# Kernel tuning notes

Hardware: AMD Instinct MI355X
Metric: run time of the kernel (lower is better)

Reference implementation:

```python
import jax, jax.numpy as jnp
import numpy as np

B, T, C, H = 4, 2048, 1024, 16
D = C // H  # head_dim = 64

def setup_inputs() -> dict:
    key = jax.random.key(0)
    k1, k2, k3 = jax.random.split(key, 3)
    x = jax.random.normal(k1, (B, T, C), dtype=jnp.float32)
    # Linear weights stored as (out_features, in_features) like torch; we apply x @ W.T
    w_attn = jax.random.normal(k2, (3 * C, C), dtype=jnp.float32) * (1.0 / np.sqrt(C))
    w_proj = jax.random.normal(k3, (C, C), dtype=jnp.float32) * (1.0 / np.sqrt(C))
    return {"x": x, "w_attn": w_attn, "w_proj": w_proj}

def reference(x, w_attn, w_proj):
    Bv, Tv, Cv = x.shape
    qkv = jnp.einsum('btc,fc->btf', x, w_attn)  # [B,T,3C]
    q, k, v = jnp.split(qkv, 3, axis=-1)
    # [B,H,T,D]
    q = q.reshape(Bv, Tv, H, D).transpose(0, 2, 1, 3)
    k = k.reshape(Bv, Tv, H, D).transpose(0, 2, 1, 3)
    v = v.reshape(Bv, Tv, H, D).transpose(0, 2, 1, 3)
    scale = 1.0 / np.sqrt(D).astype(np.float32)
    att = jnp.einsum('bhqd,bhkd->bhqk', q, k) * scale
    causal = jnp.tril(jnp.ones((Tv, Tv), dtype=bool))
    att = jnp.where(causal, att, -jnp.inf)
    att = jax.nn.softmax(att, axis=-1)
    y = jnp.einsum('bhqk,bhkd->bhqd', att, v)
    y = y.transpose(0, 2, 1, 3).reshape(Bv, Tv, Cv)
    return jnp.einsum('btc,oc->bto', y, w_proj)
```

## Files before the change

kernel.cpp:

```cpp
#include <hip/hip_runtime.h>
#include <cstdint>
#include <cstddef>

typedef __attribute__((ext_vector_type(8))) short short8;
typedef __attribute__((ext_vector_type(4))) float f32x4;
typedef unsigned int u32;

#define MFMA_BF16(a, b, c) __builtin_amdgcn_mfma_f32_16x16x32_bf16((a), (b), (c), 0, 0, 0)

__device__ __forceinline__ void async16(const void* g, void* l) {
  __builtin_amdgcn_global_load_lds(
      (const __attribute__((address_space(1))) u32*)g,
      (__attribute__((address_space(3))) u32*)l, 16, 0, 0);
}

__device__ __forceinline__ short f2bf(float f) {
  u32 u = __builtin_bit_cast(u32, f);
  u += 0x7fffu + ((u >> 16) & 1u);
  return (short)(u >> 16);
}

__device__ __forceinline__ u32 pack_bf16_trunc(float lo, float hi) {
  return __builtin_amdgcn_perm(__builtin_bit_cast(u32, hi),
                               __builtin_bit_cast(u32, lo), 0x07060302u);
}

__global__ void cast_bf16_kernel(const float* __restrict__ in,
                                 short* __restrict__ out, int n4) {
  int i = blockIdx.x * blockDim.x + threadIdx.x;
  if (i < n4) {
    float4 v = ((const float4*)in)[i];
    short4 r;
    r.x = f2bf(v.x); r.y = f2bf(v.y); r.z = f2bf(v.z); r.w = f2bf(v.w);
    ((short4*)out)[i] = r;
  }
}

__global__ void cast_wattn_kernel(const float* __restrict__ in,
                                  short* __restrict__ out, int n4) {
  int i = blockIdx.x * blockDim.x + threadIdx.x;
  if (i < n4) {
    const float sc = (i * 4 < 1024 * 1024) ? 0.18033688011112042f : 1.0f;
    float4 v = ((const float4*)in)[i];
    short4 r;
    r.x = f2bf(v.x * sc); r.y = f2bf(v.y * sc);
    r.z = f2bf(v.z * sc); r.w = f2bf(v.w * sc);
    ((short4*)out)[i] = r;
  }
}

template <bool OUT_BF16>
__global__ __launch_bounds__(256) void gemm_bt_kernel(
    const short* __restrict__ A, const short* __restrict__ Bt,
    void* __restrict__ Cv, int M, int N, int K) {
  __shared__ __align__(16) short As[128 * 32];
  __shared__ __align__(16) short Bs[128 * 32];

  const int tid  = threadIdx.x;
  const int lane = tid & 63;
  const int wave = tid >> 6;
  const int quad = lane >> 4;
  const int l15  = lane & 15;
  const int bm   = blockIdx.y * 128;
  const int bn   = blockIdx.x * 128;
  const int wm   = (wave >> 1) * 64;
  const int wn   = (wave & 1) * 64;

  f32x4 acc[4][4];
#pragma unroll
  for (int i = 0; i < 4; ++i)
#pragma unroll
    for (int j = 0; j < 4; ++j) acc[i][j] = (f32x4){0.f, 0.f, 0.f, 0.f};

  const int ci0 = tid, ci1 = tid + 256;
  const short* ga0 = A  + (size_t)(bm + (ci0 >> 2)) * K + (ci0 & 3) * 8;
  const short* ga1 = A  + (size_t)(bm + (ci1 >> 2)) * K + (ci1 & 3) * 8;
  const short* gb0 = Bt + (size_t)(bn + (ci0 >> 2)) * K + (ci0 & 3) * 8;
  const short* gb1 = Bt + (size_t)(bn + (ci1 >> 2)) * K + (ci1 & 3) * 8;

  for (int k0 = 0; k0 < K; k0 += 32) {
    __syncthreads();
    async16(ga0 + k0, &As[ci0 * 8]);
    async16(ga1 + k0, &As[ci1 * 8]);
    async16(gb0 + k0, &Bs[ci0 * 8]);
    async16(gb1 + k0, &Bs[ci1 * 8]);
    __syncthreads();

    short8 af[4], bf[4];
#pragma unroll
    for (int mt = 0; mt < 4; ++mt)
      af[mt] = *(const short8*)&As[(wm + mt * 16 + l15) * 32 + quad * 8];
#pragma unroll
    for (int nt = 0; nt < 4; ++nt)
      bf[nt] = *(const short8*)&Bs[(wn + nt * 16 + l15) * 32 + quad * 8];
#pragma unroll
    for (int mt = 0; mt < 4; ++mt)
#pragma unroll
      for (int nt = 0; nt < 4; ++nt)
        acc[mt][nt] = MFMA_BF16(af[mt], bf[nt], acc[mt][nt]);
  }

#pragma unroll
  for (int mt = 0; mt < 4; ++mt) {
    const int r0 = bm + wm + mt * 16 + quad * 4;
#pragma unroll
    for (int nt = 0; nt < 4; ++nt) {
      const int c = bn + wn + nt * 16 + l15;
#pragma unroll
      for (int reg = 0; reg < 4; ++reg) {
        float v = acc[mt][nt][reg];
        if (OUT_BF16)
          ((short*)Cv)[(size_t)(r0 + reg) * N + c] = f2bf(v);
        else
          ((float*)Cv)[(size_t)(r0 + reg) * N + c] = v;
      }
    }
  }
}

__global__ __launch_bounds__(256) void vtrans_kernel(
    const short* __restrict__ qkv, short* __restrict__ vt) {
  __shared__ __align__(16) short Ts[64 * 80];
  const int t0 = blockIdx.x * 64;
  const int bh = blockIdx.y;
  const int b = bh >> 4, h = bh & 15;
  const int tid = threadIdx.x;
#pragma unroll
  for (int it = 0; it < 2; ++it) {
    const int ci = tid + it * 256;
    const int t = ci >> 3, cw = ci & 7;
    short8 v = *(const short8*)(qkv + (size_t)(b * 2048 + t0 + t) * 3072 +
                                2048 + h * 64 + cw * 8);
    *(short8*)&Ts[t * 80 + cw * 8] = v;
  }
  __syncthreads();
#pragma unroll
  for (int it = 0; it < 2; ++it) {
    const int ci = tid + it * 256;
    const int d = ci >> 3, c2 = ci & 7;
    short tmp[8];
#pragma unroll
    for (int j = 0; j < 8; ++j) tmp[j] = Ts[(c2 * 8 + j) * 80 + d];
    *(short8*)(vt + (size_t)(bh * 64 + d) * 2048 + t0 + c2 * 8) =
        *(short8*)tmp;
  }
}

__global__ __launch_bounds__(256, 2) void attn_kernel(
    const short* __restrict__ qkv, const short* __restrict__ vt,
    short* __restrict__ y) {
  __shared__ __align__(16) short Ks[2][2 * 64 * 32];
  __shared__ __align__(16) short Vs[2][2 * 64 * 32];
  __shared__ __align__(16) short Ps[4][1024];

  const int bh    = blockIdx.x;
  const int pairi = blockIdx.y;
  const int b = bh >> 4, h = bh & 15;
  const int tid  = threadIdx.x;
  const int lane = tid & 63;
  const int wave = tid >> 6;
  const int quad = lane >> 4, l15 = lane & 15;
  const int base_row = b * 2048;
  short* Pw = &Ps[wave][0];
  const int sw = l15 & 3;

  const int ci0 = tid, ci1 = tid + 256;
  const short* kbase0 = qkv + (size_t)(base_row + ((ci0 >> 2) & 63)) * 3072 +
                        1024 + h * 64 + (ci0 >> 8) * 32 + (ci0 & 3) * 8;
  const short* kbase1 = qkv + (size_t)(base_row + ((ci1 >> 2) & 63)) * 3072 +
                        1024 + h * 64 + (ci1 >> 8) * 32 + (ci1 & 3) * 8;
  const short* vbase0 = vt + (size_t)(bh * 64 + ((ci0 >> 2) & 63)) * 2048 +
                        (ci0 >> 8) * 32 + (ci0 & 3) * 8;
  const short* vbase1 = vt + (size_t)(bh * 64 + ((ci1 >> 2) & 63)) * 2048 +
                        (ci1 >> 8) * 32 + (ci1 & 3) * 8;

  for (int half = 0; half < 2; ++half) {
    const int qi  = half ? (15 - pairi) : pairi;
    const int r0  = qi * 128;
    const int nkt = 2 * qi + 2;
    const int qg0a = r0 + wave * 32;
    const int qg0b = qg0a + 16;

    short8 qf[2][2];
#pragma unroll
    for (int g = 0; g < 2; ++g) {
      const short* qp = qkv +
          (size_t)(base_row + qg0a + g * 16 + l15) * 3072 + h * 64 + quad * 8;
      qf[g][0] = *(const short8*)qp;
      qf[g][1] = *(const short8*)(qp + 32);
    }
    float l_r[2] = {0.f, 0.f};
    f32x4 o[2][4];
#pragma unroll
    for (int g = 0; g < 2; ++g)
#pragma unroll
      for (int dt = 0; dt < 4; ++dt) o[g][dt] = (f32x4){0.f, 0.f, 0.f, 0.f};

    {
      async16(kbase0, &Ks[0][ci0 * 8]);
      async16(kbase1, &Ks[0][ci1 * 8]);
      async16(vbase0, &Vs[0][ci0 * 8]);
      async16(vbase1, &Vs[0][ci1 * 8]);
    }

    for (int kt = 0; kt < nkt; ++kt) {
      const int kvb = kt * 64;
      __syncthreads();

      if (kt + 1 < nkt) {
        const int nb = (kt + 1) & 1;
        const size_t koff = (size_t)(kvb + 64) * 3072;
        async16(kbase0 + koff, &Ks[nb][ci0 * 8]);
        async16(kbase1 + koff, &Ks[nb][ci1 * 8]);
        async16(vbase0 + kvb + 64, &Vs[nb][ci0 * 8]);
        async16(vbase1 + kvb + 64, &Vs[nb][ci1 * 8]);
      }
      const short* Kb = &Ks[kt & 1][0];
      const short* Vb = &Vs[kt & 1][0];

      if (kvb <= qg0b + 15) {
        short8 kf[4][2];
#pragma unroll
        for (int nt = 0; nt < 4; ++nt) {
          kf[nt][0] = *(const short8*)&Kb[(nt * 16 + l15) * 32 + quad * 8];
          kf[nt][1] = *(const short8*)&Kb[2048 + (nt * 16 + l15) * 32 + quad * 8];
        }
#pragma unroll
        for (int g = 0; g < 2; ++g) {
          const int qg0 = qg0a + g * 16;
          if (kvb > qg0 + 15) continue;

          f32x4 s[4];
#pragma unroll
          for (int nt = 0; nt < 4; ++nt) {
            s[nt] = MFMA_BF16(kf[nt][0], qf[g][0], ((f32x4){0.f, 0.f, 0.f, 0.f}));
            s[nt] = MFMA_BF16(kf[nt][1], qf[g][1], s[nt]);
          }

          float p[4][4];
          if (kvb + 64 <= qg0) {
#pragma unroll
            for (int nt = 0; nt < 4; ++nt)
#pragma unroll
              for (int r = 0; r < 4; ++r)
                p[nt][r] = __builtin_amdgcn_exp2f(s[nt][r]);
          } else {
            const int qrel = qg0 + l15 - kvb;
#pragma unroll
            for (int nt = 0; nt < 4; ++nt)
#pragma unroll
              for (int r = 0; r < 4; ++r) {
                const int kvl = nt * 16 + quad * 4 + r;
                p[nt][r] = (kvl <= qrel) ? __builtin_amdgcn_exp2f(s[nt][r]) : 0.f;
              }
          }

          float rs = ((p[0][0] + p[0][1]) + (p[0][2] + p[0][3])) +
                     ((p[1][0] + p[1][1]) + (p[1][2] + p[1][3])) +
                     ((p[2][0] + p[2][1]) + (p[2][2] + p[2][3])) +
                     ((p[3][0] + p[3][1]) + (p[3][2] + p[3][3]));
          rs += __shfl_xor(rs, 16);
          rs += __shfl_xor(rs, 32);
          l_r[g] += rs;

#pragma unroll
          for (int nt = 0; nt < 4; ++nt) {
            u32 w0 = pack_bf16_trunc(p[nt][0], p[nt][1]);
            u32 w1 = pack_bf16_trunc(p[nt][2], p[nt][3]);
            const int chunk = (nt & 1) * 2 + (quad >> 1);
            u32* dst = (u32*)Pw + (nt >> 1) * 256 + l15 * 16 +
                       (chunk ^ sw) * 4 + (quad & 1) * 2;
            dst[0] = w0;
            dst[1] = w1;
          }
          short8 pf0 = *(const short8*)&Pw[l15 * 32 + (quad ^ sw) * 8];
          short8 pf1 = *(const short8*)&Pw[512 + l15 * 32 + (quad ^ sw) * 8];

#pragma unroll
          for (int dt = 0; dt < 4; ++dt) {
            short8 vf0 = *(const short8*)&Vb[(dt * 16 + l15) * 32 + quad * 8];
            short8 vf1 = *(const short8*)&Vb[2048 + (dt * 16 + l15) * 32 + quad * 8];
            o[g][dt] = MFMA_BF16(vf0, pf0, o[g][dt]);
            o[g][dt] = MFMA_BF16(vf1, pf1, o[g][dt]);
          }
        }
      }
    }

#pragma unroll
    for (int g = 0; g < 2; ++g) {
      const float inv = 1.f / l_r[g];
#pragma unroll
      for (int dt = 0; dt < 4; ++dt) {
        const int d = dt * 16 + quad * 4;
        u32 w0 = pack_bf16_trunc(o[g][dt][0] * inv, o[g][dt][1] * inv);
        u32 w1 = pack_bf16_trunc(o[g][dt][2] * inv, o[g][dt][3] * inv);
        *(uint2*)&Pw[(d >> 5) * 512 + l15 * 32 + (d & 31)] = make_uint2(w0, w1);
      }
      const int qq = lane >> 2, ck = lane & 3;
      const size_t yrow = (size_t)(base_row + qg0a + g * 16 + qq);
#pragma unroll
      for (int kkd = 0; kkd < 2; ++kkd) {
        short8 vv = *(const short8*)&Pw[kkd * 512 + qq * 32 + ck * 8];
        *(short8*)(y + yrow * 1024 + h * 64 + kkd * 32 + ck * 8) = vv;
      }
    }
    __syncthreads();
  }
}

extern "C" void kernel_launch(void* const* d_in, const int* in_sizes, int n_in,
                              void* d_out, int out_size, void* d_ws,
                              size_t ws_size, hipStream_t stream) {
  const float* x  = (const float*)d_in[0];
  const float* wa = (const float*)d_in[1];
  const float* wp = (const float*)d_in[2];
  float* out = (float*)d_out;

  char* ws = (char*)d_ws;
  short* xb  = (short*)(ws + 0);
  short* wab = (short*)(ws + 16777216);
  short* wpb = (short*)(ws + 23068672);
  short* qkv = (short*)(ws + 25165824);
  short* yb  = (short*)(ws + 75497472);
  short* vtb = xb;

  cast_bf16_kernel <<<8192, 256, 0, stream>>>(x,  xb,  8388608 / 4);
  cast_wattn_kernel<<<3072, 256, 0, stream>>>(wa, wab, 3145728 / 4);
  cast_bf16_kernel <<<1024, 256, 0, stream>>>(wp, wpb, 1048576 / 4);

  gemm_bt_kernel<true><<<dim3(3072 / 128, 8192 / 128), 256, 0, stream>>>(
      xb, wab, (void*)qkv, 8192, 3072, 1024);

  vtrans_kernel<<<dim3(32, 64), 256, 0, stream>>>(qkv, vtb);

  attn_kernel<<<dim3(64, 8), 256, 0, stream>>>(qkv, vtb, yb);

  gemm_bt_kernel<false><<<dim3(1024 / 128, 8192 / 128), 256, 0, stream>>>(
      yb, wpb, (void*)out, 8192, 1024, 1024);
}
```

Before: 276.4 us.

## Reorder K/V/P shared-memory tiles to fragment-major layout and hoist V fragment loads

Changes the global-to-LDS mapping so K and V tiles land in LDS in MFMA fragment order: each quad's 16 lanes read contiguous 16-byte chunks, which removes strided row access and the XOR swizzle. The P scratch layout is changed the same way and written with one 64-bit store per tile instead of two 32-bit stores. V fragments are now loaded once per KV tile before the per-group loop rather than inside it. The causal skip guard around the whole tile is removed, and keeping all V fragments live raises register pressure.

```diff
diff --git a/kernel.cpp b/kernel.cpp
--- a/kernel.cpp
+++ b/kernel.cpp
@@ -149,8 +149,8 @@
 __global__ __launch_bounds__(256, 2) void attn_kernel(
     const short* __restrict__ qkv, const short* __restrict__ vt,
     short* __restrict__ y) {
-  __shared__ __align__(16) short Ks[2][2 * 64 * 32];
-  __shared__ __align__(16) short Vs[2][2 * 64 * 32];
+  __shared__ __align__(16) short Ks[2][4096];
+  __shared__ __align__(16) short Vs[2][4096];
   __shared__ __align__(16) short Ps[4][1024];
 
   const int bh    = blockIdx.x;
@@ -162,17 +162,16 @@
   const int quad = lane >> 4, l15 = lane & 15;
   const int base_row = b * 2048;
   short* Pw = &Ps[wave][0];
-  const int sw = l15 & 3;
 
   const int ci0 = tid, ci1 = tid + 256;
-  const short* kbase0 = qkv + (size_t)(base_row + ((ci0 >> 2) & 63)) * 3072 +
-                        1024 + h * 64 + (ci0 >> 8) * 32 + (ci0 & 3) * 8;
-  const short* kbase1 = qkv + (size_t)(base_row + ((ci1 >> 2) & 63)) * 3072 +
-                        1024 + h * 64 + (ci1 >> 8) * 32 + (ci1 & 3) * 8;
-  const short* vbase0 = vt + (size_t)(bh * 64 + ((ci0 >> 2) & 63)) * 2048 +
-                        (ci0 >> 8) * 32 + (ci0 & 3) * 8;
-  const short* vbase1 = vt + (size_t)(bh * 64 + ((ci1 >> 2) & 63)) * 2048 +
-                        (ci1 >> 8) * 32 + (ci1 & 3) * 8;
+  const int ro0 = ((ci0 >> 6) & 3) * 16 + (ci0 & 15);
+  const int ro1 = ((ci1 >> 6) & 3) * 16 + (ci1 & 15);
+  const int co0 = (ci0 >> 8) * 32 + ((ci0 >> 4) & 3) * 8;
+  const int co1 = (ci1 >> 8) * 32 + ((ci1 >> 4) & 3) * 8;
+  const short* kbase0 = qkv + (size_t)(base_row + ro0) * 3072 + 1024 + h * 64 + co0;
+  const short* kbase1 = qkv + (size_t)(base_row + ro1) * 3072 + 1024 + h * 64 + co1;
+  const short* vbase0 = vt + (size_t)(bh * 64 + ro0) * 2048 + co0;
+  const short* vbase1 = vt + (size_t)(bh * 64 + ro1) * 2048 + co1;
 
   for (int half = 0; half < 2; ++half) {
     const int qi  = half ? (15 - pairi) : pairi;
@@ -196,12 +195,10 @@
 #pragma unroll
       for (int dt = 0; dt < 4; ++dt) o[g][dt] = (f32x4){0.f, 0.f, 0.f, 0.f};
 
-    {
-      async16(kbase0, &Ks[0][ci0 * 8]);
-      async16(kbase1, &Ks[0][ci1 * 8]);
-      async16(vbase0, &Vs[0][ci0 * 8]);
-      async16(vbase1, &Vs[0][ci1 * 8]);
-    }
+    async16(kbase0, &Ks[0][ci0 * 8]);
+    async16(kbase1, &Ks[0][ci1 * 8]);
+    async16(vbase0, &Vs[0][ci0 * 8]);
+    async16(vbase1, &Vs[0][ci1 * 8]);
 
     for (int kt = 0; kt < nkt; ++kt) {
       const int kvb = kt * 64;
@@ -218,71 +215,73 @@
       const short* Kb = &Ks[kt & 1][0];
       const short* Vb = &Vs[kt & 1][0];
 
-      if (kvb <= qg0b + 15) {
-        short8 kf[4][2];
+      short8 kf[4][2];
+#pragma unroll
+      for (int nt = 0; nt < 4; ++nt) {
+        kf[nt][0] = *(const short8*)&Kb[nt * 512 + quad * 128 + l15 * 8];
+        kf[nt][1] = *(const short8*)&Kb[2048 + nt * 512 + quad * 128 + l15 * 8];
+      }
+      short8 vf[4][2];
+#pragma unroll
+      for (int dt = 0; dt < 4; ++dt) {
+        vf[dt][0] = *(const short8*)&Vb[dt * 512 + quad * 128 + l15 * 8];
+        vf[dt][1] = *(const short8*)&Vb[2048 + dt * 512 + quad * 128 + l15 * 8];
+      }
+
+#pragma unroll
+      for (int g = 0; g < 2; ++g) {
+        const int qg0 = qg0a + g * 16;
+        if (kvb > qg0 + 15) continue;
+
+        f32x4 s[4];
 #pragma unroll
         for (int nt = 0; nt < 4; ++nt) {
-          kf[nt][0] = *(const short8*)&Kb[(nt * 16 + l15) * 32 + quad * 8];
-          kf[nt][1] = *(const short8*)&Kb[2048 + (nt * 16 + l15) * 32 + quad * 8];
+          s[nt] = MFMA_BF16(kf[nt][0], qf[g][0], ((f32x4){0.f, 0.f, 0.f, 0.f}));
+          s[nt] = MFMA_BF16(kf[nt][1], qf[g][1], s[nt]);
         }
-#pragma unroll
-        for (int g = 0; g < 2; ++g) {
-          const int qg0 = qg0a + g * 16;
-          if (kvb > qg0 + 15) continue;
-
-          f32x4 s[4];
-#pragma unroll
-          for (int nt = 0; nt < 4; ++nt) {
-            s[nt] = MFMA_BF16(kf[nt][0], qf[g][0], ((f32x4){0.f, 0.f, 0.f, 0.f}));
-            s[nt] = MFMA_BF16(kf[nt][1], qf[g][1], s[nt]);
-          }
-
-          float p[4][4];
-          if (kvb + 64 <= qg0) {
-#pragma unroll
-            for (int nt = 0; nt < 4; ++nt)
-#pragma unroll
-              for (int r = 0; r < 4; ++r)
-                p[nt][r] = __builtin_amdgcn_exp2f(s[nt][r]);
-          } else {
-            const int qrel = qg0 + l15 - kvb;
-#pragma unroll
-            for (int nt = 0; nt < 4; ++nt)
-#pragma unroll
-              for (int r = 0; r < 4; ++r) {
-                const int kvl = nt * 16 + quad * 4 + r;
-                p[nt][r] = (kvl <= qrel) ? __builtin_amdgcn_exp2f(s[nt][r]) : 0.f;
-              }
-          }
-
-          float rs = ((p[0][0] + p[0][1]) + (p[0][2] + p[0][3])) +
-                     ((p[1][0] + p[1][1]) + (p[1][2] + p[1][3])) +
-                     ((p[2][0] + p[2][1]) + (p[2][2] + p[2][3])) +
-                     ((p[3][0] + p[3][1]) + (p[3][2] + p[3][3]));
-          rs += __shfl_xor(rs, 16);
-          rs += __shfl_xor(rs, 32);
-          l_r[g] += rs;
-
-#pragma unroll
-          for (int nt = 0; nt < 4; ++nt) {
-            u32 w0 = pack_bf16_trunc(p[nt][0], p[nt][1]);
-            u32 w1 = pack_bf16_trunc(p[nt][2], p[nt][3]);
-            const int chunk = (nt & 1) * 2 + (quad >> 1);
-            u32* dst = (u32*)Pw + (nt >> 1) * 256 + l15 * 16 +
-                       (chunk ^ sw) * 4 + (quad & 1) * 2;
-            dst[0] = w0;
-            dst[1] = w1;
-          }
-          short8 pf0 = *(const short8*)&Pw[l15 * 32 + (quad ^ sw) * 8];
-          short8 pf1 = *(const short8*)&Pw[512 + l15 * 32 + (quad ^ sw) * 8];
-
-#pragma unroll
-          for (int dt = 0; dt < 4; ++dt) {
-            short8 vf0 = *(const short8*)&Vb[(dt * 16 + l15) * 32 + quad * 8];
-            short8 vf1 = *(const short8*)&Vb[2048 + (dt * 16 + l15) * 32 + quad * 8];
-            o[g][dt] = MFMA_BF16(vf0, pf0, o[g][dt]);
-            o[g][dt] = MFMA_BF16(vf1, pf1, o[g][dt]);
-          }
+
+        float p[4][4];
+        if (kvb + 64 <= qg0) {
+#pragma unroll
+          for (int nt = 0; nt < 4; ++nt)
+#pragma unroll
+            for (int r = 0; r < 4; ++r)
+              p[nt][r] = __builtin_amdgcn_exp2f(s[nt][r]);
+        } else {
+          const int qrel = qg0 + l15 - kvb;
+#pragma unroll
+          for (int nt = 0; nt < 4; ++nt)
+#pragma unroll
+            for (int r = 0; r < 4; ++r) {
+              const int kvl = nt * 16 + quad * 4 + r;
+              p[nt][r] = (kvl <= qrel) ? __builtin_amdgcn_exp2f(s[nt][r]) : 0.f;
+            }
+        }
+
+        float rs = ((p[0][0] + p[0][1]) + (p[0][2] + p[0][3])) +
+                   ((p[1][0] + p[1][1]) + (p[1][2] + p[1][3])) +
+                   ((p[2][0] + p[2][1]) + (p[2][2] + p[2][3])) +
+                   ((p[3][0] + p[3][1]) + (p[3][2] + p[3][3]));
+        rs += __shfl_xor(rs, 16);
+        rs += __shfl_xor(rs, 32);
+        l_r[g] += rs;
+
+#pragma unroll
+        for (int nt = 0; nt < 4; ++nt) {
+          u32 w0 = pack_bf16_trunc(p[nt][0], p[nt][1]);
+          u32 w1 = pack_bf16_trunc(p[nt][2], p[nt][3]);
+          const int p0 = 8 * nt + 2 * quad;
+          u32* dst = (u32*)Pw + (p0 >> 4) * 256 + ((p0 >> 2) & 3) * 64 +
+                     l15 * 4 + (p0 & 3);
+          *(uint2*)dst = make_uint2(w0, w1);
+        }
+        short8 pf0 = *(const short8*)&Pw[quad * 128 + l15 * 8];
+        short8 pf1 = *(const short8*)&Pw[512 + quad * 128 + l15 * 8];
+
+#pragma unroll
+        for (int dt = 0; dt < 4; ++dt) {
+          o[g][dt] = MFMA_BF16(vf[dt][0], pf0, o[g][dt]);
+          o[g][dt] = MFMA_BF16(vf[dt][1], pf1, o[g][dt]);
         }
       }
     }
```

Result: no change. 271.4 us (-1.8%).
